# Optimization experiments

Hardware: AMD Instinct MI355X
Metric: run time of the kernel (lower is better)

Reference implementation:

```python
import jax, jax.numpy as jnp
import numpy as np

B, N, L = 1, 512, 1024
D_MSA = 64
N_HEAD = 8
D_HID = 8
LN_EPS = 1e-5


def setup_inputs() -> dict:
    key = jax.random.key(0)
    ks = jax.random.split(key, 7)
    scale = 0.05  # xavier-ish; original zero-inits to_g/to_out but random is better for testing
    return {
        "msa": jax.random.normal(ks[0], (B, N, L, D_MSA), jnp.float32),
        "ln_w": jnp.ones((D_MSA,), jnp.float32),
        "ln_b": jnp.zeros((D_MSA,), jnp.float32),
        "Wq": jax.random.normal(ks[1], (D_MSA, N_HEAD * D_HID), jnp.float32) * scale,
        "Wk": jax.random.normal(ks[2], (D_MSA, D_HID), jnp.float32) * scale,
        "Wv": jax.random.normal(ks[3], (D_MSA, D_HID), jnp.float32) * scale,
        "Wg": jax.random.normal(ks[4], (D_MSA, N_HEAD * D_HID), jnp.float32) * scale,
        "bg": jnp.ones((N_HEAD * D_HID,), jnp.float32),
        "Wo": jax.random.normal(ks[5], (N_HEAD * D_HID, D_MSA), jnp.float32) * scale,
        "bo": jnp.zeros((D_MSA,), jnp.float32),
    }


def reference(msa, ln_w, ln_b, Wq, Wk, Wv, Wg, bg, Wo, bo):
    h, dh = N_HEAD, D_HID
    scaling = 1.0 / np.sqrt(dh).astype(np.float32)
    b, n, l, d = msa.shape

    # LayerNorm over the feature dim
    mu = msa.mean(axis=-1, keepdims=True)
    var = ((msa - mu) ** 2).mean(axis=-1, keepdims=True)
    x = (msa - mu) * jax.lax.rsqrt(var + LN_EPS) * ln_w + ln_b  # [b,n,l,d]

    # projections
    q = (x @ Wq).reshape(b, n, l, h, dh).mean(axis=1) * scaling  # [b,l,h,dh] mean-pooled query
    k = x @ Wk  # [b,n,l,dh] shared across heads
    v = x @ Wv  # [b,n,l,dh]
    gate = jax.nn.sigmoid(x @ Wg + bg)  # [b,n,l,h*dh]

    # global column attention: attend over the N (sequence) axis per residue column
    attn = jax.nn.softmax(jnp.einsum("blhd,bnld->blhn", q, k), axis=-1)  # [b,l,h,n]
    out = jnp.einsum("blhn,bnld->blhd", attn, v).reshape(b, 1, l, h * dh)

    out = gate * out  # broadcast over N -> [b,n,l,h*dh]
    return out @ Wo + bo  # [b,n,l,d_msa]
```

## Files before the change

kernel.cpp:

```cpp
#include <hip/hip_runtime.h>


#define NN 512
#define LL 1024
#define DD 64

typedef float fx4 __attribute__((ext_vector_type(4)));
typedef unsigned int ux2 __attribute__((ext_vector_type(2)));
typedef short bh8 __attribute__((ext_vector_type(8)));

__device__ __forceinline__ unsigned short f2bf(float f) {
  union { float f; unsigned int u; } c; c.f = f;
  unsigned int u = c.u;
  u += 0x7fffu + ((u >> 16) & 1u);
  return (unsigned short)(u >> 16);
}
__device__ __forceinline__ float bf2f(unsigned short b) {
  union { unsigned int u; float f; } c; c.u = ((unsigned int)b) << 16;
  return c.f;
}

__global__ __launch_bounds__(256) void k1_kernel(
    const float* __restrict__ msa, const float* __restrict__ lnw,
    const float* __restrict__ lnb, const float* __restrict__ Wk,
    const float* __restrict__ Wv, unsigned short* __restrict__ wsK,
    unsigned short* __restrict__ wsV, float* __restrict__ wsXsumP)
{
  const int tid = threadIdx.x;
  const int w = tid >> 6;
  const int lane = tid & 63;
  const int p = lane >> 4;
  const int f = lane & 15;
  const int lq = blockIdx.x >> 2;
  const int nr = blockIdx.x & 3;
  const int l = (lq << 2) + p;
  const int n0 = (nr << 7) + (w << 5);

  fx4 lw = *(const fx4*)(lnw + 4 * f);
  fx4 lb = *(const fx4*)(lnb + 4 * f);

  float wk[4][8], wvv[4][8];
#pragma unroll
  for (int i = 0; i < 4; ++i)
#pragma unroll
    for (int j = 0; j < 8; ++j) {
      wk[i][j]  = Wk[(4 * f + i) * 8 + j];
      wvv[i][j] = Wv[(4 * f + i) * 8 + j];
    }

  fx4 xs = {0.f, 0.f, 0.f, 0.f};

  for (int it = 0; it < 32; ++it) {
    int n = n0 + it;
    fx4 x = *(const fx4*)(msa + ((size_t)n * LL + l) * DD + 4 * f);
    float s  = x.x + x.y + x.z + x.w;
    float ss = x.x * x.x + x.y * x.y + x.z * x.z + x.w * x.w;
#pragma unroll
    for (int m = 1; m <= 8; m <<= 1) {
      s  += __shfl_xor(s, m);
      ss += __shfl_xor(ss, m);
    }
    float mu  = s * (1.f / 64.f);
    float var = ss * (1.f / 64.f) - mu * mu;
    float rs  = rsqrtf(var + 1e-5f);
    fx4 xn;
    xn.x = (x.x - mu) * rs * lw.x + lb.x;
    xn.y = (x.y - mu) * rs * lw.y + lb.y;
    xn.z = (x.z - mu) * rs * lw.z + lb.z;
    xn.w = (x.w - mu) * rs * lw.w + lb.w;
    xs += xn;

    float kp[8], vp[8];
#pragma unroll
    for (int j = 0; j < 8; ++j) {
      kp[j] = xn.x * wk[0][j];
      kp[j] = fmaf(xn.y, wk[1][j], kp[j]);
      kp[j] = fmaf(xn.z, wk[2][j], kp[j]);
      kp[j] = fmaf(xn.w, wk[3][j], kp[j]);
      vp[j] = xn.x * wvv[0][j];
      vp[j] = fmaf(xn.y, wvv[1][j], vp[j]);
      vp[j] = fmaf(xn.z, wvv[2][j], vp[j]);
      vp[j] = fmaf(xn.w, wvv[3][j], vp[j]);
    }
#pragma unroll
    for (int m = 1; m <= 8; m <<= 1) {
#pragma unroll
      for (int j = 0; j < 8; ++j) {
        kp[j] += __shfl_xor(kp[j], m);
        vp[j] += __shfl_xor(vp[j], m);
      }
    }
    float kv = kp[0], vv2 = vp[0];
#pragma unroll
    for (int j = 1; j < 8; ++j) {
      if (f == j) { kv = kp[j]; vv2 = vp[j]; }
    }
    if (f < 8) {
      size_t off = ((size_t)l * NN + n) * 8 + f;
      wsK[off] = f2bf(kv);
      wsV[off] = f2bf(vv2);
    }
  }

  __shared__ float xred[4][4][64];
  *(fx4*)&xred[w][p][4 * f] = xs;
  __syncthreads();
  int pp = tid >> 6, ff = tid & 63;
  float v4 = xred[0][pp][ff] + xred[1][pp][ff] + xred[2][pp][ff] + xred[3][pp][ff];
  wsXsumP[(size_t)nr * (LL * 64) + ((lq << 2) + pp) * 64 + ff] = v4;
}

__global__ __launch_bounds__(256) void k2_kernel(
    const float* __restrict__ Wq, const float* __restrict__ wsXsumP,
    const unsigned short* __restrict__ wsK, const unsigned short* __restrict__ wsV,
    float* __restrict__ wsAttn)
{
  __shared__ float red[4][32][65];
  const int tid = threadIdx.x;
  const int w = tid >> 6;
  const int lane = tid & 63;
  const int l = (blockIdx.x << 2) + w;

  float xl = wsXsumP[l * 64 + lane]
           + wsXsumP[1 * (LL * 64) + l * 64 + lane]
           + wsXsumP[2 * (LL * 64) + l * 64 + lane]
           + wsXsumP[3 * (LL * 64) + l * 64 + lane];
  float acc = 0.f;
#pragma unroll
  for (int d = 0; d < 64; ++d) {
    float xd = __shfl(xl, d);
    acc = fmaf(xd, Wq[d * 64 + lane], acc);
  }
  float qq = acc * (1.f / 512.f) * 0.35355339059327373f;
  float qv[64];
#pragma unroll
  for (int j = 0; j < 64; ++j) qv[j] = __shfl(qq, j);

  float s[8][8];
  const unsigned short* kb = wsK + (size_t)l * NN * 8;
#pragma unroll
  for (int c = 0; c < 8; ++c) {
    int n = (c << 6) + lane;
    uint4 kr = *(const uint4*)(kb + n * 8);
    float kf[8];
    kf[0] = bf2f((unsigned short)(kr.x & 0xffffu)); kf[1] = bf2f((unsigned short)(kr.x >> 16));
    kf[2] = bf2f((unsigned short)(kr.y & 0xffffu)); kf[3] = bf2f((unsigned short)(kr.y >> 16));
    kf[4] = bf2f((unsigned short)(kr.z & 0xffffu)); kf[5] = bf2f((unsigned short)(kr.z >> 16));
    kf[6] = bf2f((unsigned short)(kr.w & 0xffffu)); kf[7] = bf2f((unsigned short)(kr.w >> 16));
#pragma unroll
    for (int h = 0; h < 8; ++h) {
      float t = 0.f;
#pragma unroll
      for (int dh = 0; dh < 8; ++dh) t = fmaf(qv[h * 8 + dh], kf[dh], t);
      s[c][h] = t;
    }
  }

  float mx[8];
#pragma unroll
  for (int h = 0; h < 8; ++h) mx[h] = s[0][h];
#pragma unroll
  for (int c = 1; c < 8; ++c)
#pragma unroll
    for (int h = 0; h < 8; ++h) mx[h] = fmaxf(mx[h], s[c][h]);
#pragma unroll
  for (int m = 1; m < 64; m <<= 1)
#pragma unroll
    for (int h = 0; h < 8; ++h) mx[h] = fmaxf(mx[h], __shfl_xor(mx[h], m));

  float den[8] = {0.f, 0.f, 0.f, 0.f, 0.f, 0.f, 0.f, 0.f};
#pragma unroll
  for (int c = 0; c < 8; ++c)
#pragma unroll
    for (int h = 0; h < 8; ++h) { s[c][h] = __expf(s[c][h] - mx[h]); den[h] += s[c][h]; }
#pragma unroll
  for (int m = 1; m < 64; m <<= 1)
#pragma unroll
    for (int h = 0; h < 8; ++h) den[h] += __shfl_xor(den[h], m);
  float rden[8];
#pragma unroll
  for (int h = 0; h < 8; ++h) rden[h] = 1.f / den[h];

  float oa[64];
#pragma unroll
  for (int j = 0; j < 64; ++j) oa[j] = 0.f;
  const unsigned short* vb = wsV + (size_t)l * NN * 8;
#pragma unroll
  for (int c = 0; c < 8; ++c) {
    int n = (c << 6) + lane;
    uint4 vr = *(const uint4*)(vb + n * 8);
    float vf[8];
    vf[0] = bf2f((unsigned short)(vr.x & 0xffffu)); vf[1] = bf2f((unsigned short)(vr.x >> 16));
    vf[2] = bf2f((unsigned short)(vr.y & 0xffffu)); vf[3] = bf2f((unsigned short)(vr.y >> 16));
    vf[4] = bf2f((unsigned short)(vr.z & 0xffffu)); vf[5] = bf2f((unsigned short)(vr.z >> 16));
    vf[6] = bf2f((unsigned short)(vr.w & 0xffffu)); vf[7] = bf2f((unsigned short)(vr.w >> 16));
#pragma unroll
    for (int h = 0; h < 8; ++h) {
      float pch = s[c][h];
#pragma unroll
      for (int dh = 0; dh < 8; ++dh) oa[h * 8 + dh] = fmaf(pch, vf[dh], oa[h * 8 + dh]);
    }
  }
#pragma unroll
  for (int h = 0; h < 8; ++h)
#pragma unroll
    for (int dh = 0; dh < 8; ++dh) oa[h * 8 + dh] *= rden[h];

  float o0 = 0.f, o1 = 0.f;
#pragma unroll
  for (int j = 0; j < 32; ++j) red[w][j][lane] = oa[j];
#pragma unroll
  for (int src = 0; src < 64; ++src) o0 += red[w][lane & 31][src];
#pragma unroll
  for (int j = 0; j < 32; ++j) red[w][j][lane] = oa[32 + j];
#pragma unroll
  for (int src = 0; src < 64; ++src) o1 += red[w][lane & 31][src];
  if (lane < 32) {
    wsAttn[l * 64 + lane] = o0;
    wsAttn[l * 64 + 32 + lane] = o1;
  }
}

__global__ __launch_bounds__(256) void k3_kernel(
    const float* __restrict__ msa, const float* __restrict__ lnw,
    const float* __restrict__ lnb, const float* __restrict__ Wg,
    const float* __restrict__ bg, const float* __restrict__ Wo,
    const float* __restrict__ bo, const float* __restrict__ wsAttn,
    float* __restrict__ outp)
{
  __shared__ unsigned short xt[256][64];
  __shared__ unsigned short wgT[64][64];
  __shared__ unsigned short woT[64][64];
  __shared__ unsigned short yt[4][16][64];

  const int tid = threadIdx.x;
  const int w = tid >> 6;
  const int lane = tid & 63;

  {
    int d = tid & 63;
    int jg = tid >> 6;
#pragma unroll
    for (int j0 = 0; j0 < 16; ++j0) {
      int j = (j0 << 2) + jg;
      int gs = ((d >> 3) ^ (j & 7)) * 8 + (d & 7);
      wgT[j][gs] = f2bf(Wg[d * 64 + j]);
      woT[j][gs] = f2bf(Wo[d * 64 + j]);
    }
  }

  const int ps = lane >> 4, f = lane & 15;
  fx4 lw = *(const fx4*)(lnw + 4 * f);
  fx4 lb = *(const fx4*)(lnb + 4 * f);
  const size_t gbase = (size_t)blockIdx.x * 256;
  for (int it = 0; it < 16; ++it) {
    int posL = (w << 6) + (it << 2) + ps;
    size_t gpos = gbase + posL;
    fx4 x = *(const fx4*)(msa + gpos * 64 + 4 * f);
    float sv  = x.x + x.y + x.z + x.w;
    float ssv = x.x * x.x + x.y * x.y + x.z * x.z + x.w * x.w;
#pragma unroll
    for (int m = 1; m <= 8; m <<= 1) { sv += __shfl_xor(sv, m); ssv += __shfl_xor(ssv, m); }
    float mu  = sv * (1.f / 64.f);
    float var = ssv * (1.f / 64.f) - mu * mu;
    float rs  = rsqrtf(var + 1e-5f);
    float x0 = (x.x - mu) * rs * lw.x + lb.x;
    float x1 = (x.y - mu) * rs * lw.y + lb.y;
    float x2 = (x.z - mu) * rs * lw.z + lb.z;
    float x3 = (x.w - mu) * rs * lw.w + lb.w;
    unsigned int u0 = (unsigned int)f2bf(x0) | ((unsigned int)f2bf(x1) << 16);
    unsigned int u1 = (unsigned int)f2bf(x2) | ((unsigned int)f2bf(x3) << 16);
    int gsw = (((f >> 1) ^ (posL & 7)) * 8) + (f & 1) * 4;
    ux2 uu = {u0, u1};
    *(ux2*)&xt[posL][gsw] = uu;
  }
  __syncthreads();

  const int c  = lane & 15;
  const int kg = lane >> 4;
  bh8 bgf[4][2], bof[4][2];
  float bgv[4], bov[4];
#pragma unroll
  for (int nt = 0; nt < 4; ++nt) {
    int col = (nt << 4) + c;
    int sw = col & 7;
    bgf[nt][0] = *(const bh8*)&wgT[col][((kg    ) ^ sw) * 8];
    bgf[nt][1] = *(const bh8*)&wgT[col][((kg + 4) ^ sw) * 8];
    bof[nt][0] = *(const bh8*)&woT[col][((kg    ) ^ sw) * 8];
    bof[nt][1] = *(const bh8*)&woT[col][((kg + 4) ^ sw) * 8];
    bgv[nt] = bg[col];
    bov[nt] = bo[col];
  }

  const int lbase = (int)(gbase & (LL - 1));
  fx4 zero = {0.f, 0.f, 0.f, 0.f};
#pragma unroll
  for (int mt = 0; mt < 4; ++mt) {
    int r0 = (w << 6) + (mt << 4);
    int rowA = r0 + c;
    int swA = rowA & 7;
    bh8 a0 = *(const bh8*)&xt[rowA][((kg    ) ^ swA) * 8];
    bh8 a1 = *(const bh8*)&xt[rowA][((kg + 4) ^ swA) * 8];
    fx4 ag[4];
#pragma unroll
    for (int nt = 0; nt < 4; ++nt) {
      fx4 t = __builtin_amdgcn_mfma_f32_16x16x32_bf16(a0, bgf[nt][0], zero, 0, 0, 0);
      ag[nt] = __builtin_amdgcn_mfma_f32_16x16x32_bf16(a1, bgf[nt][1], t, 0, 0, 0);
    }
#pragma unroll
    for (int nt = 0; nt < 4; ++nt) {
      int col = (nt << 4) + c;
#pragma unroll
      for (int r = 0; r < 4; ++r) {
        int rloc = (kg << 2) + r;
        float z = ag[nt][r] + bgv[nt];
        float g = 1.f / (1.f + __expf(-z));
        int lidx = lbase + r0 + rloc;
        float a = wsAttn[lidx * 64 + col];
        float y = g * a;
        int gy = (((col >> 3) ^ (rloc & 7)) * 8) + (col & 7);
        yt[w][rloc][gy] = f2bf(y);
      }
    }
    int swY = c & 7;
    bh8 y0 = *(const bh8*)&yt[w][c][((kg    ) ^ swY) * 8];
    bh8 y1 = *(const bh8*)&yt[w][c][((kg + 4) ^ swY) * 8];
    fx4 ao[4];
#pragma unroll
    for (int nt = 0; nt < 4; ++nt) {
      fx4 t = __builtin_amdgcn_mfma_f32_16x16x32_bf16(y0, bof[nt][0], zero, 0, 0, 0);
      ao[nt] = __builtin_amdgcn_mfma_f32_16x16x32_bf16(y1, bof[nt][1], t, 0, 0, 0);
    }
#pragma unroll
    for (int nt = 0; nt < 4; ++nt) {
      int col = (nt << 4) + c;
#pragma unroll
      for (int r = 0; r < 4; ++r) {
        int rloc = (kg << 2) + r;
        size_t gpos = gbase + r0 + rloc;
        outp[gpos * 64 + col] = ao[nt][r] + bov[nt];
      }
    }
  }
}

extern "C" void kernel_launch(void* const* d_in, const int* in_sizes, int n_in,
                              void* d_out, int out_size, void* d_ws, size_t ws_size,
                              hipStream_t stream) {
  const float* msa = (const float*)d_in[0];
  const float* lnw = (const float*)d_in[1];
  const float* lnb = (const float*)d_in[2];
  const float* Wq  = (const float*)d_in[3];
  const float* Wk  = (const float*)d_in[4];
  const float* Wv  = (const float*)d_in[5];
  const float* Wg  = (const float*)d_in[6];
  const float* bg  = (const float*)d_in[7];
  const float* Wo  = (const float*)d_in[8];
  const float* bo  = (const float*)d_in[9];
  float* outp = (float*)d_out;

  char* ws = (char*)d_ws;
  unsigned short* wsK    = (unsigned short*)ws;
  unsigned short* wsV    = (unsigned short*)(ws + 8388608);
  float*          wsXsum = (float*)(ws + 16777216);
  float*          wsAttn = (float*)(ws + 17825792);

  k1_kernel<<<dim3(1024), dim3(256), 0, stream>>>(msa, lnw, lnb, Wk, Wv, wsK, wsV, wsXsum);
  k2_kernel<<<dim3(256),  dim3(256), 0, stream>>>(Wq, wsXsum, wsK, wsV, wsAttn);
  k3_kernel<<<dim3(2048), dim3(256), 0, stream>>>(msa, lnw, lnb, Wg, bg, Wo, bo, wsAttn, outp);
}
```

Measured before the change: 390.7 us.

## Use MFMA for K/V projection, interleave KV layout, parallelize attention per head

K1 now computes the K and V projections with bf16 MFMA over 16x16 tiles instead of scalar FMAs and shuffle reductions, and writes K and V interleaved in one buffer. Its partial sums now come from 32 N-chunks instead of 4. K2 launches one 512-thread block per residue with one wave per head, shrinking per-thread register arrays and dropping the LDS reduction. K3 restructures LayerNorm into per-wave 16-row tiles with double-buffered LDS, cutting shared memory use. The aim is less ALU and register pressure and better occupancy, at the cost of more partial-sum traffic and more complexity.

```diff
diff --git a/kernel.cpp b/kernel.cpp
--- a/kernel.cpp
+++ b/kernel.cpp
@@ -3,19 +3,18 @@
 
 #define NN 512
 #define LL 1024
-#define DD 64
 
 typedef float fx4 __attribute__((ext_vector_type(4)));
 typedef unsigned int ux2 __attribute__((ext_vector_type(2)));
 typedef short bh8 __attribute__((ext_vector_type(8)));
 
-__device__ __forceinline__ unsigned short f2bf(float f) {
+static __device__ __forceinline__ unsigned short f2bf(float f) {
   union { float f; unsigned int u; } c; c.f = f;
   unsigned int u = c.u;
   u += 0x7fffu + ((u >> 16) & 1u);
   return (unsigned short)(u >> 16);
 }
-__device__ __forceinline__ float bf2f(unsigned short b) {
+static __device__ __forceinline__ float bf2f(unsigned short b) {
   union { unsigned int u; float f; } c; c.u = ((unsigned int)b) << 16;
   return c.f;
 }
@@ -23,201 +22,208 @@
 __global__ __launch_bounds__(256) void k1_kernel(
     const float* __restrict__ msa, const float* __restrict__ lnw,
     const float* __restrict__ lnb, const float* __restrict__ Wk,
-    const float* __restrict__ Wv, unsigned short* __restrict__ wsK,
-    unsigned short* __restrict__ wsV, float* __restrict__ wsXsumP)
+    const float* __restrict__ Wv, unsigned short* __restrict__ wsKV,
+    float* __restrict__ wsXsumP)
 {
+  __shared__ unsigned short wkv[16][64];
+  __shared__ unsigned short xt[4][2][16][64];
+  __shared__ float xsred[4][16][64];
+
+  const int tid  = threadIdx.x;
+  const int w    = tid >> 6;
+  const int lane = tid & 63;
+  const int p    = lane >> 4;
+  const int f    = lane & 15;
+  const int nb   = blockIdx.x >> 6;
+  const int lbk  = blockIdx.x & 63;
+  const int n0   = nb << 4;
+  const int l0   = lbk << 4;
+
+  {
+    const int col = tid & 15;
+    const int d0  = (tid >> 4) << 2;
+    const float* Wsrc = (col < 8) ? Wk : Wv;
+    const int cc = col & 7;
+#pragma unroll
+    for (int dd = 0; dd < 4; ++dd) {
+      const int d  = d0 + dd;
+      const int gs = (((d >> 3) ^ (col & 7)) << 3) + (d & 7);
+      wkv[col][gs] = f2bf(Wsrc[d * 8 + cc]);
+    }
+  }
+  __syncthreads();
+
+  const int c  = lane & 15;
+  const int kg = lane >> 4;
+  const bh8 wb0 = *(const bh8*)&wkv[c][((kg    ) ^ (c & 7)) << 3];
+  const bh8 wb1 = *(const bh8*)&wkv[c][((kg + 4) ^ (c & 7)) << 3];
+
+  const fx4 lwv = *(const fx4*)(lnw + 4 * f);
+  const fx4 lbv = *(const fx4*)(lnb + 4 * f);
+  const fx4 zero = {0.f, 0.f, 0.f, 0.f};
+
+  fx4 xs4[4];
+#pragma unroll
+  for (int jq = 0; jq < 4; ++jq) { xs4[jq].x = 0.f; xs4[jq].y = 0.f; xs4[jq].z = 0.f; xs4[jq].w = 0.f; }
+
+#pragma unroll
+  for (int it = 0; it < 4; ++it) {
+    const int i = (w << 2) + it;
+    const int n = n0 + i;
+    const int bufp = it & 1;
+#pragma unroll
+    for (int jq = 0; jq < 4; ++jq) {
+      const int j = (jq << 2) + p;
+      fx4 x = *(const fx4*)(msa + ((size_t)n * LL + (l0 + j)) * 64 + 4 * f);
+      float s  = x.x + x.y + x.z + x.w;
+      float ss = x.x * x.x + x.y * x.y + x.z * x.z + x.w * x.w;
+#pragma unroll
+      for (int m = 1; m <= 8; m <<= 1) { s += __shfl_xor(s, m); ss += __shfl_xor(ss, m); }
+      const float mu  = s * (1.f / 64.f);
+      const float var = ss * (1.f / 64.f) - mu * mu;
+      const float rs  = rsqrtf(var + 1e-5f);
+      fx4 xn;
+      xn.x = (x.x - mu) * rs * lwv.x + lbv.x;
+      xn.y = (x.y - mu) * rs * lwv.y + lbv.y;
+      xn.z = (x.z - mu) * rs * lwv.z + lbv.z;
+      xn.w = (x.w - mu) * rs * lwv.w + lbv.w;
+      xs4[jq] += xn;
+      const unsigned int u0 = (unsigned int)f2bf(xn.x) | ((unsigned int)f2bf(xn.y) << 16);
+      const unsigned int u1 = (unsigned int)f2bf(xn.z) | ((unsigned int)f2bf(xn.w) << 16);
+      const int gsw = (((f >> 1) ^ (j & 7)) << 3) + ((f & 1) << 2);
+      ux2 uu = {u0, u1};
+      *(ux2*)&xt[w][bufp][j][gsw] = uu;
+    }
+    bh8 a0 = *(const bh8*)&xt[w][bufp][c][((kg    ) ^ (c & 7)) << 3];
+    bh8 a1 = *(const bh8*)&xt[w][bufp][c][((kg + 4) ^ (c & 7)) << 3];
+    fx4 kv = __builtin_amdgcn_mfma_f32_16x16x32_bf16(a0, wb0, zero, 0, 0, 0);
+    kv = __builtin_amdgcn_mfma_f32_16x16x32_bf16(a1, wb1, kv, 0, 0, 0);
+#pragma unroll
+    for (int r = 0; r < 4; ++r) {
+      const int l = l0 + (kg << 2) + r;
+      wsKV[((size_t)l * NN + n) * 16 + c] = f2bf(kv[r]);
+    }
+  }
+
+#pragma unroll
+  for (int jq = 0; jq < 4; ++jq)
+    *(fx4*)&xsred[w][(jq << 2) + p][4 * f] = xs4[jq];
+  __syncthreads();
+  {
+    const int j  = tid >> 4;
+    const int fq = tid & 15;
+    fx4 a  = *(const fx4*)&xsred[0][j][4 * fq];
+    fx4 b  = *(const fx4*)&xsred[1][j][4 * fq];
+    fx4 c2 = *(const fx4*)&xsred[2][j][4 * fq];
+    fx4 d  = *(const fx4*)&xsred[3][j][4 * fq];
+    fx4 ssum = (a + b) + (c2 + d);
+    *(fx4*)(wsXsumP + ((size_t)nb * LL + (l0 + j)) * 64 + 4 * fq) = ssum;
+  }
+}
+
+__global__ __launch_bounds__(512) void k2_kernel(
+    const float* __restrict__ Wq, const float* __restrict__ wsXsumP,
+    const unsigned short* __restrict__ wsKV, float* __restrict__ wsAttn)
+{
+  __shared__ float xsp[8][64];
+  __shared__ float xsum[64];
   const int tid = threadIdx.x;
-  const int w = tid >> 6;
+  const int l   = blockIdx.x;
+
+  {
+    const int d  = tid & 63;
+    const int c0 = tid >> 6;
+    float acc = 0.f;
+#pragma unroll
+    for (int m = 0; m < 4; ++m)
+      acc += wsXsumP[((size_t)(c0 + (m << 3)) * LL + l) * 64 + d];
+    xsp[c0][d] = acc;
+  }
+  __syncthreads();
+  if (tid < 64) {
+    float a = 0.f;
+#pragma unroll
+    for (int cg = 0; cg < 8; ++cg) a += xsp[cg][tid];
+    xsum[tid] = a;
+  }
+  __syncthreads();
+
+  const int h    = tid >> 6;
   const int lane = tid & 63;
-  const int p = lane >> 4;
-  const int f = lane & 15;
-  const int lq = blockIdx.x >> 2;
-  const int nr = blockIdx.x & 3;
-  const int l = (lq << 2) + p;
-  const int n0 = (nr << 7) + (w << 5);
-
-  fx4 lw = *(const fx4*)(lnw + 4 * f);
-  fx4 lb = *(const fx4*)(lnb + 4 * f);
-
-  float wk[4][8], wvv[4][8];
-#pragma unroll
-  for (int i = 0; i < 4; ++i)
-#pragma unroll
-    for (int j = 0; j < 8; ++j) {
-      wk[i][j]  = Wk[(4 * f + i) * 8 + j];
-      wvv[i][j] = Wv[(4 * f + i) * 8 + j];
-    }
-
-  fx4 xs = {0.f, 0.f, 0.f, 0.f};
-
-  for (int it = 0; it < 32; ++it) {
-    int n = n0 + it;
-    fx4 x = *(const fx4*)(msa + ((size_t)n * LL + l) * DD + 4 * f);
-    float s  = x.x + x.y + x.z + x.w;
-    float ss = x.x * x.x + x.y * x.y + x.z * x.z + x.w * x.w;
-#pragma unroll
-    for (int m = 1; m <= 8; m <<= 1) {
-      s  += __shfl_xor(s, m);
-      ss += __shfl_xor(ss, m);
-    }
-    float mu  = s * (1.f / 64.f);
-    float var = ss * (1.f / 64.f) - mu * mu;
-    float rs  = rsqrtf(var + 1e-5f);
-    fx4 xn;
-    xn.x = (x.x - mu) * rs * lw.x + lb.x;
-    xn.y = (x.y - mu) * rs * lw.y + lb.y;
-    xn.z = (x.z - mu) * rs * lw.z + lb.z;
-    xn.w = (x.w - mu) * rs * lw.w + lb.w;
-    xs += xn;
-
-    float kp[8], vp[8];
-#pragma unroll
-    for (int j = 0; j < 8; ++j) {
-      kp[j] = xn.x * wk[0][j];
-      kp[j] = fmaf(xn.y, wk[1][j], kp[j]);
-      kp[j] = fmaf(xn.z, wk[2][j], kp[j]);
-      kp[j] = fmaf(xn.w, wk[3][j], kp[j]);
-      vp[j] = xn.x * wvv[0][j];
-      vp[j] = fmaf(xn.y, wvv[1][j], vp[j]);
-      vp[j] = fmaf(xn.z, wvv[2][j], vp[j]);
-      vp[j] = fmaf(xn.w, wvv[3][j], vp[j]);
-    }
-#pragma unroll
-    for (int m = 1; m <= 8; m <<= 1) {
-#pragma unroll
-      for (int j = 0; j < 8; ++j) {
-        kp[j] += __shfl_xor(kp[j], m);
-        vp[j] += __shfl_xor(vp[j], m);
-      }
-    }
-    float kv = kp[0], vv2 = vp[0];
-#pragma unroll
-    for (int j = 1; j < 8; ++j) {
-      if (f == j) { kv = kp[j]; vv2 = vp[j]; }
-    }
-    if (f < 8) {
-      size_t off = ((size_t)l * NN + n) * 8 + f;
-      wsK[off] = f2bf(kv);
-      wsV[off] = f2bf(vv2);
-    }
-  }
-
-  __shared__ float xred[4][4][64];
-  *(fx4*)&xred[w][p][4 * f] = xs;
-  __syncthreads();
-  int pp = tid >> 6, ff = tid & 63;
-  float v4 = xred[0][pp][ff] + xred[1][pp][ff] + xred[2][pp][ff] + xred[3][pp][ff];
-  wsXsumP[(size_t)nr * (LL * 64) + ((lq << 2) + pp) * 64 + ff] = v4;
-}
-
-__global__ __launch_bounds__(256) void k2_kernel(
-    const float* __restrict__ Wq, const float* __restrict__ wsXsumP,
-    const unsigned short* __restrict__ wsK, const unsigned short* __restrict__ wsV,
-    float* __restrict__ wsAttn)
-{
-  __shared__ float red[4][32][65];
-  const int tid = threadIdx.x;
-  const int w = tid >> 6;
-  const int lane = tid & 63;
-  const int l = (blockIdx.x << 2) + w;
-
-  float xl = wsXsumP[l * 64 + lane]
-           + wsXsumP[1 * (LL * 64) + l * 64 + lane]
-           + wsXsumP[2 * (LL * 64) + l * 64 + lane]
-           + wsXsumP[3 * (LL * 64) + l * 64 + lane];
-  float acc = 0.f;
-#pragma unroll
-  for (int d = 0; d < 64; ++d) {
-    float xd = __shfl(xl, d);
-    acc = fmaf(xd, Wq[d * 64 + lane], acc);
-  }
-  float qq = acc * (1.f / 512.f) * 0.35355339059327373f;
-  float qv[64];
-#pragma unroll
-  for (int j = 0; j < 64; ++j) qv[j] = __shfl(qq, j);
-
-  float s[8][8];
-  const unsigned short* kb = wsK + (size_t)l * NN * 8;
-#pragma unroll
-  for (int c = 0; c < 8; ++c) {
-    int n = (c << 6) + lane;
-    uint4 kr = *(const uint4*)(kb + n * 8);
-    float kf[8];
-    kf[0] = bf2f((unsigned short)(kr.x & 0xffffu)); kf[1] = bf2f((unsigned short)(kr.x >> 16));
-    kf[2] = bf2f((unsigned short)(kr.y & 0xffffu)); kf[3] = bf2f((unsigned short)(kr.y >> 16));
-    kf[4] = bf2f((unsigned short)(kr.z & 0xffffu)); kf[5] = bf2f((unsigned short)(kr.z >> 16));
-    kf[6] = bf2f((unsigned short)(kr.w & 0xffffu)); kf[7] = bf2f((unsigned short)(kr.w >> 16));
-#pragma unroll
-    for (int h = 0; h < 8; ++h) {
-      float t = 0.f;
-#pragma unroll
-      for (int dh = 0; dh < 8; ++dh) t = fmaf(qv[h * 8 + dh], kf[dh], t);
-      s[c][h] = t;
-    }
-  }
-
-  float mx[8];
-#pragma unroll
-  for (int h = 0; h < 8; ++h) mx[h] = s[0][h];
-#pragma unroll
-  for (int c = 1; c < 8; ++c)
-#pragma unroll
-    for (int h = 0; h < 8; ++h) mx[h] = fmaxf(mx[h], s[c][h]);
+  const int dh   = lane & 7;
+  const int g    = lane >> 3;
+
+  float qp = 0.f;
+#pragma unroll
+  for (int k = 0; k < 8; ++k) {
+    const int d = (g << 3) + k;
+    qp = fmaf(xsum[d], Wq[d * 64 + (h << 3) + dh], qp);
+  }
+  qp += __shfl_xor(qp, 8);
+  qp += __shfl_xor(qp, 16);
+  qp += __shfl_xor(qp, 32);
+  const float qsc = qp * (0.35355339059327373f / 512.f);
+  float qv[8];
+#pragma unroll
+  for (int j2 = 0; j2 < 8; ++j2) qv[j2] = __shfl(qsc, j2);
+
+  const unsigned short* kvb = wsKV + (size_t)l * NN * 16;
+  float s[8];
+#pragma unroll
+  for (int cc = 0; cc < 8; ++cc) {
+    const int n = (cc << 6) + lane;
+    uint4 kr = *(const uint4*)(kvb + (size_t)n * 16);
+    float t;
+    t = qv[0] * bf2f((unsigned short)(kr.x & 0xffffu));
+    t = fmaf(qv[1], bf2f((unsigned short)(kr.x >> 16)), t);
+    t = fmaf(qv[2], bf2f((unsigned short)(kr.y & 0xffffu)), t);
+    t = fmaf(qv[3], bf2f((unsigned short)(kr.y >> 16)), t);
+    t = fmaf(qv[4], bf2f((unsigned short)(kr.z & 0xffffu)), t);
+    t = fmaf(qv[5], bf2f((unsigned short)(kr.z >> 16)), t);
+    t = fmaf(qv[6], bf2f((unsigned short)(kr.w & 0xffffu)), t);
+    t = fmaf(qv[7], bf2f((unsigned short)(kr.w >> 16)), t);
+    s[cc] = t;
+  }
+  float mx = s[0];
+#pragma unroll
+  for (int cc = 1; cc < 8; ++cc) mx = fmaxf(mx, s[cc]);
+#pragma unroll
+  for (int m = 1; m < 64; m <<= 1) mx = fmaxf(mx, __shfl_xor(mx, m));
+  float den = 0.f;
+#pragma unroll
+  for (int cc = 0; cc < 8; ++cc) { s[cc] = __expf(s[cc] - mx); den += s[cc]; }
+#pragma unroll
+  for (int m = 1; m < 64; m <<= 1) den += __shfl_xor(den, m);
+  const float rden = 1.f / den;
+
+  float oa[8];
+#pragma unroll
+  for (int j2 = 0; j2 < 8; ++j2) oa[j2] = 0.f;
+#pragma unroll
+  for (int cc = 0; cc < 8; ++cc) {
+    const int n = (cc << 6) + lane;
+    uint4 vr = *(const uint4*)(kvb + (size_t)n * 16 + 8);
+    const float pch = s[cc];
+    oa[0] = fmaf(pch, bf2f((unsigned short)(vr.x & 0xffffu)), oa[0]);
+    oa[1] = fmaf(pch, bf2f((unsigned short)(vr.x >> 16)), oa[1]);
+    oa[2] = fmaf(pch, bf2f((unsigned short)(vr.y & 0xffffu)), oa[2]);
+    oa[3] = fmaf(pch, bf2f((unsigned short)(vr.y >> 16)), oa[3]);
+    oa[4] = fmaf(pch, bf2f((unsigned short)(vr.z & 0xffffu)), oa[4]);
+    oa[5] = fmaf(pch, bf2f((unsigned short)(vr.z >> 16)), oa[5]);
+    oa[6] = fmaf(pch, bf2f((unsigned short)(vr.w & 0xffffu)), oa[6]);
+    oa[7] = fmaf(pch, bf2f((unsigned short)(vr.w >> 16)), oa[7]);
+  }
+#pragma unroll
+  for (int j2 = 0; j2 < 8; ++j2) oa[j2] *= rden;
 #pragma unroll
   for (int m = 1; m < 64; m <<= 1)
 #pragma unroll
-    for (int h = 0; h < 8; ++h) mx[h] = fmaxf(mx[h], __shfl_xor(mx[h], m));
-
-  float den[8] = {0.f, 0.f, 0.f, 0.f, 0.f, 0.f, 0.f, 0.f};
-#pragma unroll
-  for (int c = 0; c < 8; ++c)
-#pragma unroll
-    for (int h = 0; h < 8; ++h) { s[c][h] = __expf(s[c][h] - mx[h]); den[h] += s[c][h]; }
-#pragma unroll
-  for (int m = 1; m < 64; m <<= 1)
-#pragma unroll
-    for (int h = 0; h < 8; ++h) den[h] += __shfl_xor(den[h], m);
-  float rden[8];
-#pragma unroll
-  for (int h = 0; h < 8; ++h) rden[h] = 1.f / den[h];
-
-  float oa[64];
-#pragma unroll
-  for (int j = 0; j < 64; ++j) oa[j] = 0.f;
-  const unsigned short* vb = wsV + (size_t)l * NN * 8;
-#pragma unroll
-  for (int c = 0; c < 8; ++c) {
-    int n = (c << 6) + lane;
-    uint4 vr = *(const uint4*)(vb + n * 8);
-    float vf[8];
-    vf[0] = bf2f((unsigned short)(vr.x & 0xffffu)); vf[1] = bf2f((unsigned short)(vr.x >> 16));
-    vf[2] = bf2f((unsigned short)(vr.y & 0xffffu)); vf[3] = bf2f((unsigned short)(vr.y >> 16));
-    vf[4] = bf2f((unsigned short)(vr.z & 0xffffu)); vf[5] = bf2f((unsigned short)(vr.z >> 16));
-    vf[6] = bf2f((unsigned short)(vr.w & 0xffffu)); vf[7] = bf2f((unsigned short)(vr.w >> 16));
-#pragma unroll
-    for (int h = 0; h < 8; ++h) {
-      float pch = s[c][h];
-#pragma unroll
-      for (int dh = 0; dh < 8; ++dh) oa[h * 8 + dh] = fmaf(pch, vf[dh], oa[h * 8 + dh]);
-    }
-  }
-#pragma unroll
-  for (int h = 0; h < 8; ++h)
-#pragma unroll
-    for (int dh = 0; dh < 8; ++dh) oa[h * 8 + dh] *= rden[h];
-
-  float o0 = 0.f, o1 = 0.f;
-#pragma unroll
-  for (int j = 0; j < 32; ++j) red[w][j][lane] = oa[j];
-#pragma unroll
-  for (int src = 0; src < 64; ++src) o0 += red[w][lane & 31][src];
-#pragma unroll
-  for (int j = 0; j < 32; ++j) red[w][j][lane] = oa[32 + j];
-#pragma unroll
-  for (int src = 0; src < 64; ++src) o1 += red[w][lane & 31][src];
-  if (lane < 32) {
-    wsAttn[l * 64 + lane] = o0;
-    wsAttn[l * 64 + 32 + lane] = o1;
+    for (int j2 = 0; j2 < 8; ++j2) oa[j2] += __shfl_xor(oa[j2], m);
+  if (lane < 8) {
+    float ov = oa[0];
+#pragma unroll
+    for (int j2 = 1; j2 < 8; ++j2) if (lane == j2) ov = oa[j2];
+    wsAttn[l * 64 + (h << 3) + lane] = ov;
   }
 }
 
@@ -228,117 +234,115 @@
     const float* __restrict__ bo, const float* __restrict__ wsAttn,
     float* __restrict__ outp)
 {
-  __shared__ unsigned short xt[256][64];
   __shared__ unsigned short wgT[64][64];
   __shared__ unsigned short woT[64][64];
+  __shared__ unsigned short xt[4][2][16][64];
   __shared__ unsigned short yt[4][16][64];
 
-  const int tid = threadIdx.x;
-  const int w = tid >> 6;
+  const int tid  = threadIdx.x;
+  const int w    = tid >> 6;
   const int lane = tid & 63;
 
   {
-    int d = tid & 63;
-    int jg = tid >> 6;
+    const int d  = tid & 63;
+    const int jg = tid >> 6;
 #pragma unroll
     for (int j0 = 0; j0 < 16; ++j0) {
-      int j = (j0 << 2) + jg;
-      int gs = ((d >> 3) ^ (j & 7)) * 8 + (d & 7);
+      const int j  = (j0 << 2) + jg;
+      const int gs = (((d >> 3) ^ (j & 7)) << 3) + (d & 7);
       wgT[j][gs] = f2bf(Wg[d * 64 + j]);
       woT[j][gs] = f2bf(Wo[d * 64 + j]);
     }
   }
-
-  const int ps = lane >> 4, f = lane & 15;
-  fx4 lw = *(const fx4*)(lnw + 4 * f);
-  fx4 lb = *(const fx4*)(lnb + 4 * f);
-  const size_t gbase = (size_t)blockIdx.x * 256;
-  for (int it = 0; it < 16; ++it) {
-    int posL = (w << 6) + (it << 2) + ps;
-    size_t gpos = gbase + posL;
-    fx4 x = *(const fx4*)(msa + gpos * 64 + 4 * f);
-    float sv  = x.x + x.y + x.z + x.w;
-    float ssv = x.x * x.x + x.y * x.y + x.z * x.z + x.w * x.w;
-#pragma unroll
-    for (int m = 1; m <= 8; m <<= 1) { sv += __shfl_xor(sv, m); ssv += __shfl_xor(ssv, m); }
-    float mu  = sv * (1.f / 64.f);
-    float var = ssv * (1.f / 64.f) - mu * mu;
-    float rs  = rsqrtf(var + 1e-5f);
-    float x0 = (x.x - mu) * rs * lw.x + lb.x;
-    float x1 = (x.y - mu) * rs * lw.y + lb.y;
-    float x2 = (x.z - mu) * rs * lw.z + lb.z;
-    float x3 = (x.w - mu) * rs * lw.w + lb.w;
-    unsigned int u0 = (unsigned int)f2bf(x0) | ((unsigned int)f2bf(x1) << 16);
-    unsigned int u1 = (unsigned int)f2bf(x2) | ((unsigned int)f2bf(x3) << 16);
-    int gsw = (((f >> 1) ^ (posL & 7)) * 8) + (f & 1) * 4;
-    ux2 uu = {u0, u1};
-    *(ux2*)&xt[posL][gsw] = uu;
-  }
   __syncthreads();
 
   const int c  = lane & 15;
   const int kg = lane >> 4;
-  bh8 bgf[4][2], bof[4][2];
+  const int p  = lane >> 4;
+  const int f  = lane & 15;
+
+  bh8 bgf0[4], bgf1[4], bof0[4], bof1[4];
   float bgv[4], bov[4];
 #pragma unroll
   for (int nt = 0; nt < 4; ++nt) {
-    int col = (nt << 4) + c;
-    int sw = col & 7;
-    bgf[nt][0] = *(const bh8*)&wgT[col][((kg    ) ^ sw) * 8];
-    bgf[nt][1] = *(const bh8*)&wgT[col][((kg + 4) ^ sw) * 8];
-    bof[nt][0] = *(const bh8*)&woT[col][((kg    ) ^ sw) * 8];
-    bof[nt][1] = *(const bh8*)&woT[col][((kg + 4) ^ sw) * 8];
+    const int col = (nt << 4) + c;
+    const int sw  = col & 7;
+    bgf0[nt] = *(const bh8*)&wgT[col][((kg    ) ^ sw) << 3];
+    bgf1[nt] = *(const bh8*)&wgT[col][((kg + 4) ^ sw) << 3];
+    bof0[nt] = *(const bh8*)&woT[col][((kg    ) ^ sw) << 3];
+    bof1[nt] = *(const bh8*)&woT[col][((kg + 4) ^ sw) << 3];
     bgv[nt] = bg[col];
     bov[nt] = bo[col];
   }
 
-  const int lbase = (int)(gbase & (LL - 1));
-  fx4 zero = {0.f, 0.f, 0.f, 0.f};
-#pragma unroll
-  for (int mt = 0; mt < 4; ++mt) {
-    int r0 = (w << 6) + (mt << 4);
-    int rowA = r0 + c;
-    int swA = rowA & 7;
-    bh8 a0 = *(const bh8*)&xt[rowA][((kg    ) ^ swA) * 8];
-    bh8 a1 = *(const bh8*)&xt[rowA][((kg + 4) ^ swA) * 8];
+  const fx4 lwv = *(const fx4*)(lnw + 4 * f);
+  const fx4 lbv = *(const fx4*)(lnb + 4 * f);
+  const fx4 zero = {0.f, 0.f, 0.f, 0.f};
+
+#pragma unroll
+  for (int it = 0; it < 4; ++it) {
+    const int Tg = (blockIdx.x << 4) + (w << 2) + it;
+    const size_t pb = (size_t)Tg << 4;
+    const int bufp = it & 1;
+#pragma unroll
+    for (int jq = 0; jq < 4; ++jq) {
+      const int j = (jq << 2) + p;
+      fx4 x = *(const fx4*)(msa + (pb + j) * 64 + 4 * f);
+      float s  = x.x + x.y + x.z + x.w;
+      float ss = x.x * x.x + x.y * x.y + x.z * x.z + x.w * x.w;
+#pragma unroll
+      for (int m = 1; m <= 8; m <<= 1) { s += __shfl_xor(s, m); ss += __shfl_xor(ss, m); }
+      const float mu  = s * (1.f / 64.f);
+      const float var = ss * (1.f / 64.f) - mu * mu;
+      const float rs  = rsqrtf(var + 1e-5f);
+      const float x0 = (x.x - mu) * rs * lwv.x + lbv.x;
+      const float x1 = (x.y - mu) * rs * lwv.y + lbv.y;
+      const float x2 = (x.z - mu) * rs * lwv.z + lbv.z;
+      const float x3 = (x.w - mu) * rs * lwv.w + lbv.w;
+      const unsigned int u0 = (unsigned int)f2bf(x0) | ((unsigned int)f2bf(x1) << 16);
+      const unsigned int u1 = (unsigned int)f2bf(x2) | ((unsigned int)f2bf(x3) << 16);
+      const int gsw = (((f >> 1) ^ (j & 7)) << 3) + ((f & 1) << 2);
+      ux2 uu = {u0, u1};
+      *(ux2*)&xt[w][bufp][j][gsw] = uu;
+    }
+    bh8 a0 = *(const bh8*)&xt[w][bufp][c][((kg    ) ^ (c & 7)) << 3];
+    bh8 a1 = *(const bh8*)&xt[w][bufp][c][((kg + 4) ^ (c & 7)) << 3];
     fx4 ag[4];
 #pragma unroll
     for (int nt = 0; nt < 4; ++nt) {
-      fx4 t = __builtin_amdgcn_mfma_f32_16x16x32_bf16(a0, bgf[nt][0], zero, 0, 0, 0);
-      ag[nt] = __builtin_amdgcn_mfma_f32_16x16x32_bf16(a1, bgf[nt][1], t, 0, 0, 0);
-    }
+      fx4 t = __builtin_amdgcn_mfma_f32_16x16x32_bf16(a0, bgf0[nt], zero, 0, 0, 0);
+      ag[nt] = __builtin_amdgcn_mfma_f32_16x16x32_bf16(a1, bgf1[nt], t, 0, 0, 0);
+    }
+    const int lb2 = (int)(pb & (LL - 1));
 #pragma unroll
     for (int nt = 0; nt < 4; ++nt) {
-      int col = (nt << 4) + c;
+      const int col = (nt << 4) + c;
 #pragma unroll
       for (int r = 0; r < 4; ++r) {
-        int rloc = (kg << 2) + r;
-        float z = ag[nt][r] + bgv[nt];
-        float g = 1.f / (1.f + __expf(-z));
-        int lidx = lbase + r0 + rloc;
-        float a = wsAttn[lidx * 64 + col];
-        float y = g * a;
-        int gy = (((col >> 3) ^ (rloc & 7)) * 8) + (col & 7);
+        const int rloc = (kg << 2) + r;
+        const float z  = ag[nt][r] + bgv[nt];
+        const float gt = 1.f / (1.f + __expf(-z));
+        const float av = wsAttn[(lb2 + rloc) * 64 + col];
+        const float y  = gt * av;
+        const int gy = (((col >> 3) ^ (rloc & 7)) << 3) + (col & 7);
         yt[w][rloc][gy] = f2bf(y);
       }
     }
-    int swY = c & 7;
-    bh8 y0 = *(const bh8*)&yt[w][c][((kg    ) ^ swY) * 8];
-    bh8 y1 = *(const bh8*)&yt[w][c][((kg + 4) ^ swY) * 8];
+    bh8 y0 = *(const bh8*)&yt[w][c][((kg    ) ^ (c & 7)) << 3];
+    bh8 y1 = *(const bh8*)&yt[w][c][((kg + 4) ^ (c & 7)) << 3];
     fx4 ao[4];
 #pragma unroll
     for (int nt = 0; nt < 4; ++nt) {
-      fx4 t = __builtin_amdgcn_mfma_f32_16x16x32_bf16(y0, bof[nt][0], zero, 0, 0, 0);
-      ao[nt] = __builtin_amdgcn_mfma_f32_16x16x32_bf16(y1, bof[nt][1], t, 0, 0, 0);
+      fx4 t = __builtin_amdgcn_mfma_f32_16x16x32_bf16(y0, bof0[nt], zero, 0, 0, 0);
+      ao[nt] = __builtin_amdgcn_mfma_f32_16x16x32_bf16(y1, bof1[nt], t, 0, 0, 0);
     }
 #pragma unroll
     for (int nt = 0; nt < 4; ++nt) {
-      int col = (nt << 4) + c;
+      const int col = (nt << 4) + c;
 #pragma unroll
       for (int r = 0; r < 4; ++r) {
-        int rloc = (kg << 2) + r;
-        size_t gpos = gbase + r0 + rloc;
-        outp[gpos * 64 + col] = ao[nt][r] + bov[nt];
+        const int rloc = (kg << 2) + r;
+        outp[(pb + rloc) * 64 + col] = ao[nt][r] + bov[nt];
       }
     }
   }
@@ -360,12 +364,11 @@
   float* outp = (float*)d_out;
 
   char* ws = (char*)d_ws;
-  unsigned short* wsK    = (unsigned short*)ws;
-  unsigned short* wsV    = (unsigned short*)(ws + 8388608);
-  float*          wsXsum = (float*)(ws + 16777216);
-  float*          wsAttn = (float*)(ws + 17825792);
-
-  k1_kernel<<<dim3(1024), dim3(256), 0, stream>>>(msa, lnw, lnb, Wk, Wv, wsK, wsV, wsXsum);
-  k2_kernel<<<dim3(256),  dim3(256), 0, stream>>>(Wq, wsXsum, wsK, wsV, wsAttn);
+  unsigned short* wsKV    = (unsigned short*)ws;
+  float*          wsXsumP = (float*)(ws + 16777216);
+  float*          wsAttn  = (float*)(ws + 25165824);
+
+  k1_kernel<<<dim3(2048), dim3(256), 0, stream>>>(msa, lnw, lnb, Wk, Wv, wsKV, wsXsumP);
+  k2_kernel<<<dim3(1024), dim3(512), 0, stream>>>(Wq, wsXsumP, wsKV, wsAttn);
   k3_kernel<<<dim3(2048), dim3(256), 0, stream>>>(msa, lnw, lnb, Wg, bg, Wo, bo, wsAttn, outp);
 }
```

New measurement: 354.0 us. -9.4%, faster.
